# Kernel tuning notes

Measured on AMD Instinct MI355X. Metric: run time of the kernel, lower is better.

The kernel has to match this reference:

```python
import jax, jax.numpy as jnp
import numpy as np

N = 50000   # nodes
E = 400000  # edges
IN = 128    # in_dim
D = 32      # out_dim (per head)
H = 8       # heads
M = 8       # random features; must equal H so m//heads == 1 (see notes)


def setup_inputs() -> dict:
    key = jax.random.key(0)
    ks = jax.random.split(key, 8)
    x = jax.random.normal(ks[0], (N, IN), dtype=jnp.float32)
    edge_index = jax.random.randint(ks[1], (2, E), 0, N, dtype=jnp.int32)
    edge_sign = (2 * jax.random.randint(ks[2], (E,), 0, 2, dtype=jnp.int32) - 1)  # {-1,+1}
    s = 1.0 / np.sqrt(IN)
    Wq = jax.random.normal(ks[3], (IN, H * D), dtype=jnp.float32) * s
    Wk = jax.random.normal(ks[4], (IN, H * D), dtype=jnp.float32) * s
    Wv = jax.random.normal(ks[5], (IN, H * D), dtype=jnp.float32) * s
    RF = jax.random.normal(ks[6], (D, M), dtype=jnp.float32)    # iSKDE buffer
    RF_q = jax.random.normal(ks[7], (D, M), dtype=jnp.float32)  # frozen param
    return {"x": x, "Wq": Wq, "Wk": Wk, "Wv": Wv, "RF": RF, "RF_q": RF_q,
            "edge_index": edge_index, "edge_sign": edge_sign}


def reference(x, Wq, Wk, Wv, RF, RF_q, edge_index, edge_sign):
    n = x.shape[0]
    q = (x @ Wq).reshape(n, H, D)
    k = (x @ Wk).reshape(n, H, D)
    v = (x @ Wv).reshape(n, H, D)

    # ---- iSKDE.build (torch.no_grad) over N*H 'nodes' (rows of k_flat) ----
    k_flat = k.reshape(n * H, D)
    proj = k_flat @ RF                                  # [N*H, M]
    phi = (jnp.cos(proj) + jnp.sin(proj)).reshape(n * H, H, M // H)  # [N*H, H, 1]

    src, dst = edge_index[0], edge_index[1]
    posf = (edge_sign == 1).astype(x.dtype)             # [E]
    negf = (edge_sign == -1).astype(x.dtype)

    deg_pos = jnp.zeros((n * H, H), x.dtype).at[dst].add(jnp.broadcast_to(posf[:, None], (E, H)))
    deg_neg = jnp.zeros((n * H, H), x.dtype).at[dst].add(jnp.broadcast_to(negf[:, None], (E, H)))
    phi_src = phi[src]                                  # [E, H, 1]
    pk_pos = jnp.zeros((n * H, H, M // H), x.dtype).at[dst].add(phi_src * posf[:, None, None])
    pk_neg = jnp.zeros((n * H, H, M // H), x.dtype).at[dst].add(phi_src * negf[:, None, None])
    # build is under torch.no_grad -> constants w.r.t. autodiff
    pk_pos, pk_neg, deg_pos, deg_neg = map(jax.lax.stop_gradient, (pk_pos, pk_neg, deg_pos, deg_neg))

    # ---- random-feature query map ----
    qproj = q @ RF_q                                    # [N, H, M]
    q_phi = jnp.cos(qproj) + jnp.sin(qproj)

    # ---- iSKDE.forward on edges (row=src queries, col=dst keys) ----
    q_e = q_phi[src]                                    # [E, H, M]
    num_pos = (q_e * pk_pos[dst]).sum(-1)               # [E,H,M]*[E,H,1] -> [E,H]
    num_neg = (q_e * pk_neg[dst]).sum(-1)
    den_pos = jnp.maximum(deg_pos[dst], 1.0)            # clamp_min(1)
    den_neg = jnp.maximum(deg_neg[dst], 1.0)

    attn = jax.nn.softmax(num_pos / den_pos, axis=-1) - jax.nn.softmax(num_neg / den_neg, axis=-1)
    # dropout p=0.0 -> identity

    messages = v[dst] * attn[..., None]                 # [E, H, D]
    out = jnp.zeros((n, H, D), x.dtype).at[src].add(messages)
    return out.reshape(n, -1)
```

## Files before the change

kernel.cpp:

```cpp
#include <hip/hip_runtime.h>

constexpr int N_NODES = 50000;
constexpr int E_EDGES = 400000;
constexpr int IN_DIM  = 128;
constexpr int HD      = 256;
constexpr int H_HEADS = 8;
constexpr int D_HEAD  = 32;
constexpr int M_FEAT  = 8;
constexpr int K_NODES = N_NODES / H_HEADS;
constexpr int CAP     = 48;
constexpr int BUCKET_BLOCKS = (E_EDGES + 255) / 256;
constexpr int XFORM_BLOCKS  = N_NODES / 16;
constexpr int ZERO_INT4     = (2 * N_NODES) / 4;
constexpr int ZERO_BLOCKS   = (ZERO_INT4 + 255) / 256;

typedef __attribute__((ext_vector_type(8))) short bf16x8;
typedef __attribute__((ext_vector_type(4))) float f32x4;

__device__ inline short to_bf16(float f) {
    unsigned u = __builtin_bit_cast(unsigned, f);
    u += 0x7FFFu + ((u >> 16) & 1u);
    return (short)(u >> 16);
}
__device__ inline float bf16f(short h) {
    return __builtin_bit_cast(float, (unsigned)(unsigned short)h << 16);
}

__global__ __launch_bounds__(256) void prep_kernel(
    const float* __restrict__ Wq, const float* __restrict__ Wk,
    const float* __restrict__ Wv, const float* __restrict__ RF,
    const float* __restrict__ RFq,
    unsigned short* __restrict__ WqTh, unsigned short* __restrict__ WqTl,
    unsigned short* __restrict__ WkTh, unsigned short* __restrict__ WkTl,
    unsigned short* __restrict__ WvT, int* __restrict__ cnts)
{
    const int b = blockIdx.x;
    const int t = threadIdx.x;
    if (b < 64) {
        const bool isQ = (b < 32);
        const int idx = (isQ ? b : b - 32) * 256 + t;
        const int d = idx >> 6;
        const int c = idx & 63;
        const int hj = c >> 3, m = c & 7;
        const float* W = isQ ? Wq : Wk;
        const float* R = isQ ? RFq : RF;
        float acc = 0.f;
        #pragma unroll
        for (int dd = 0; dd < D_HEAD; ++dd)
            acc = fmaf(W[d * HD + hj * D_HEAD + dd], R[dd * M_FEAT + m], acc);
        const short h = to_bf16(acc);
        const short l = to_bf16(acc - bf16f(h));
        (isQ ? WqTh : WkTh)[c * IN_DIM + d] = (unsigned short)h;
        (isQ ? WqTl : WkTl)[c * IN_DIM + d] = (unsigned short)l;
    } else if (b < 192) {
        const int idx = (b - 64) * 256 + t;
        const int n = idx >> 7;
        const int d = idx & 127;
        WvT[idx] = (unsigned short)to_bf16(Wv[d * HD + n]);
    } else {
        const int idx = (b - 192) * 256 + t;
        if (idx < ZERO_INT4)
            ((int4*)cnts)[idx] = make_int4(0, 0, 0, 0);
    }
}

__global__ __launch_bounds__(256, 4) void main_kernel(
    const int* __restrict__ src, const int* __restrict__ dst,
    const int* __restrict__ sign,
    int* __restrict__ srcCnt, unsigned short* __restrict__ srcBucket,
    int* __restrict__ dstCnt, unsigned* __restrict__ dstBucket,
    const float* __restrict__ x, const unsigned short* __restrict__ WvT,
    const unsigned short* __restrict__ WqTh, const unsigned short* __restrict__ WqTl,
    const unsigned short* __restrict__ WkTh, const unsigned short* __restrict__ WkTl,
    unsigned short* __restrict__ Vb, float* __restrict__ Sq, float* __restrict__ Phi)
{
    if (blockIdx.x < BUCKET_BLOCKS) {
        const int e = blockIdx.x * 256 + threadIdx.x;
        if (e >= E_EDGES) return;
        const int s = src[e];
        const int d = dst[e];
        const unsigned sb = (sign[e] == 1) ? 0x80000000u : 0u;
        const int ss = atomicAdd(&srcCnt[s], 1);
        const int ds = atomicAdd(&dstCnt[d], 1);
        if (ss < CAP) srcBucket[(size_t)s * CAP + ss] = (unsigned short)d;
        if (ds < CAP) dstBucket[(size_t)d * CAP + ds] = (unsigned)s | sb;
        return;
    }

    const int r0   = (blockIdx.x - BUCKET_BLOCKS) * 16;
    const int w    = threadIdx.x >> 6;
    const int lane = threadIdx.x & 63;
    const int m    = lane & 15;
    const int quad = lane >> 4;

    bf16x8 Ah[4], Al[4];
    const float* xrow = x + (size_t)(r0 + m) * IN_DIM;
    #pragma unroll
    for (int t = 0; t < 4; ++t) {
        const float4 a = *(const float4*)(xrow + t * 32 + quad * 8);
        const float4 b = *(const float4*)(xrow + t * 32 + quad * 8 + 4);
        float vals[8] = {a.x, a.y, a.z, a.w, b.x, b.y, b.z, b.w};
        bf16x8 fh, fl;
        #pragma unroll
        for (int e = 0; e < 8; ++e) {
            const short hh = to_bf16(vals[e]);
            fh[e] = hh;
            fl[e] = to_bf16(vals[e] - bf16f(hh));
        }
        Ah[t] = fh; Al[t] = fl;
    }

    const unsigned short* bp = WvT + (size_t)m * IN_DIM + quad * 8;
    #pragma unroll
    for (int ii = 0; ii < 2; ++ii) {
        bf16x8 Bv[8];
        #pragma unroll
        for (int i = 0; i < 2; ++i) {
            const unsigned short* bc =
                bp + (size_t)(w * 4 + ii * 2 + i) * 16 * IN_DIM;
            #pragma unroll
            for (int t = 0; t < 4; ++t)
                Bv[i * 4 + t] = *(const bf16x8*)(bc + t * 32);
        }
        #pragma unroll
        for (int i = 0; i < 2; ++i) {
            const int ct = w * 4 + ii * 2 + i;
            f32x4 acc = {0.f, 0.f, 0.f, 0.f};
            #pragma unroll
            for (int t = 0; t < 4; ++t)
                acc = __builtin_amdgcn_mfma_f32_16x16x32_bf16(Ah[t], Bv[i * 4 + t], acc, 0, 0, 0);
            #pragma unroll
            for (int r = 0; r < 4; ++r)
                Vb[(size_t)(r0 + quad * 4 + r) * HD + ct * 16 + m] =
                    (unsigned short)to_bf16(acc[r]);
        }
    }

    {
        const int c = w * 16 + m;
        const unsigned short* bh = WqTh + (size_t)c * IN_DIM + quad * 8;
        const unsigned short* bl = WqTl + (size_t)c * IN_DIM + quad * 8;
        bf16x8 Bh[4], Bl[4];
        #pragma unroll
        for (int t = 0; t < 4; ++t) {
            Bh[t] = *(const bf16x8*)(bh + t * 32);
            Bl[t] = *(const bf16x8*)(bl + t * 32);
        }
        f32x4 acc1 = {0.f, 0.f, 0.f, 0.f};
        f32x4 acc2 = {0.f, 0.f, 0.f, 0.f};
        #pragma unroll
        for (int t = 0; t < 4; ++t) {
            acc1 = __builtin_amdgcn_mfma_f32_16x16x32_bf16(Ah[t], Bh[t], acc1, 0, 0, 0);
            acc2 = __builtin_amdgcn_mfma_f32_16x16x32_bf16(Al[t], Bh[t], acc2, 0, 0, 0);
        }
        #pragma unroll
        for (int t = 0; t < 4; ++t)
            acc1 = __builtin_amdgcn_mfma_f32_16x16x32_bf16(Ah[t], Bl[t], acc1, 0, 0, 0);
        #pragma unroll
        for (int r = 0; r < 4; ++r) {
            const float pv = acc1[r] + acc2[r];
            float tv = __cosf(pv) + __sinf(pv);
            tv += __shfl_xor(tv, 1);
            tv += __shfl_xor(tv, 2);
            tv += __shfl_xor(tv, 4);
            if ((lane & 7) == 0) {
                const int h = w * 2 + (m >> 3);
                Sq[(r0 + quad * 4 + r) * H_HEADS + h] = tv;
            }
        }
    }

    if (r0 < K_NODES) {
        const int c = w * 16 + m;
        const unsigned short* bh = WkTh + (size_t)c * IN_DIM + quad * 8;
        const unsigned short* bl = WkTl + (size_t)c * IN_DIM + quad * 8;
        bf16x8 Bh[4], Bl[4];
        #pragma unroll
        for (int t = 0; t < 4; ++t) {
            Bh[t] = *(const bf16x8*)(bh + t * 32);
            Bl[t] = *(const bf16x8*)(bl + t * 32);
        }
        f32x4 acc1 = {0.f, 0.f, 0.f, 0.f};
        f32x4 acc2 = {0.f, 0.f, 0.f, 0.f};
        #pragma unroll
        for (int t = 0; t < 4; ++t) {
            acc1 = __builtin_amdgcn_mfma_f32_16x16x32_bf16(Ah[t], Bh[t], acc1, 0, 0, 0);
            acc2 = __builtin_amdgcn_mfma_f32_16x16x32_bf16(Al[t], Bh[t], acc2, 0, 0, 0);
        }
        #pragma unroll
        for (int t = 0; t < 4; ++t)
            acc1 = __builtin_amdgcn_mfma_f32_16x16x32_bf16(Ah[t], Bl[t], acc1, 0, 0, 0);
        #pragma unroll
        for (int r = 0; r < 4; ++r) {
            const int row = r0 + quad * 4 + r;
            if (row < K_NODES) {
                const float pv = acc1[r] + acc2[r];
                Phi[(size_t)row * 64 + c] = __cosf(pv) + __sinf(pv);
            }
        }
    }
}

__global__ __launch_bounds__(256) void pk_kernel(
    const int* __restrict__ dstCnt, const unsigned* __restrict__ dstBucket,
    const float* __restrict__ Phi, float* __restrict__ PK)
{
    const int t = blockIdx.x * 256 + threadIdx.x;
    if (t >= N_NODES * H_HEADS) return;
    const int d = t >> 3;
    const int h = t & 7;
    int deg = dstCnt[d];
    if (deg > CAP) deg = CAP;

    float accp = 0.f, accn = 0.f;
    int cp = 0, cn = 0;
    for (int i = 0; i < deg; ++i) {
        const unsigned entry = dstBucket[(size_t)d * CAP + i];
        const float phi = Phi[(int)(entry & 0x7FFFFFFFu) * H_HEADS + h];
        if (entry & 0x80000000u) { accp += phi; ++cp; }
        else                     { accn += phi; ++cn; }
    }
    float2 pn;
    pn.x = accp / fmaxf((float)cp, 1.0f);
    pn.y = accn / fmaxf((float)cn, 1.0f);
    ((float2*)PK)[d * 8 + h] = pn;
}

__global__ __launch_bounds__(256) void accum_kernel(
    const int* __restrict__ srcCnt, const unsigned short* __restrict__ srcBucket,
    const float* __restrict__ Sq, const float* __restrict__ PK,
    const unsigned short* __restrict__ Vb, float* __restrict__ out)
{
    const int s = blockIdx.x * 4 + (threadIdx.x >> 6);
    const int lane = threadIdx.x & 63;
    const int j = lane >> 3;
    const int h = lane & 7;
    const int myhead = lane >> 3;

    int deg = srcCnt[s];
    if (deg > CAP) deg = CAP;
    const float sq = Sq[s * H_HEADS + h];

    float4 acc = make_float4(0.f, 0.f, 0.f, 0.f);
    const ushort4* __restrict__ V4 = (const ushort4*)Vb;
    const float2* __restrict__ PK2 = (const float2*)PK;

    for (int base = 0; base < deg; base += 8) {
        const int idx = base + j;
        const bool act = (idx < deg);
        const int dj = act ? (int)srcBucket[s * CAP + idx] : 0;

        const float2 pn = PK2[dj * 8 + h];
        const float np = sq * pn.x;
        const float nn = sq * pn.y;

        float mp = np, mn = nn;
        mp = fmaxf(mp, __shfl_xor(mp, 1)); mn = fmaxf(mn, __shfl_xor(mn, 1));
        mp = fmaxf(mp, __shfl_xor(mp, 2)); mn = fmaxf(mn, __shfl_xor(mn, 2));
        mp = fmaxf(mp, __shfl_xor(mp, 4)); mn = fmaxf(mn, __shfl_xor(mn, 4));
        float ep = __expf(np - mp), en = __expf(nn - mn);
        float sp = ep, sn = en;
        sp += __shfl_xor(sp, 1); sn += __shfl_xor(sn, 1);
        sp += __shfl_xor(sp, 2); sn += __shfl_xor(sn, 2);
        sp += __shfl_xor(sp, 4); sn += __shfl_xor(sn, 4);
        float a = ep / sp - en / sn;
        if (!act) a = 0.f;

        int   dd[8];
        float av[8];
        #pragma unroll
        for (int jj = 0; jj < 8; ++jj) {
            dd[jj] = __shfl(dj, jj * 8);
            av[jj] = __shfl(a,  jj * 8 + myhead);
        }
        ushort4 vv[8];
        #pragma unroll
        for (int jj = 0; jj < 8; ++jj)
            vv[jj] = V4[dd[jj] * 64 + lane];
        #pragma unroll
        for (int jj = 0; jj < 8; ++jj) {
            acc.x = fmaf(bf16f((short)vv[jj].x), av[jj], acc.x);
            acc.y = fmaf(bf16f((short)vv[jj].y), av[jj], acc.y);
            acc.z = fmaf(bf16f((short)vv[jj].z), av[jj], acc.z);
            acc.w = fmaf(bf16f((short)vv[jj].w), av[jj], acc.w);
        }
    }
    ((float4*)out)[s * 64 + lane] = acc;
}

extern "C" void kernel_launch(void* const* d_in, const int* in_sizes, int n_in,
                              void* d_out, int out_size, void* d_ws, size_t ws_size,
                              hipStream_t stream) {
    const float* x   = (const float*)d_in[0];
    const float* Wq  = (const float*)d_in[1];
    const float* Wk  = (const float*)d_in[2];
    const float* Wv  = (const float*)d_in[3];
    const float* RF  = (const float*)d_in[4];
    const float* RFq = (const float*)d_in[5];
    const int* eidx  = (const int*)d_in[6];
    const int* esign = (const int*)d_in[7];
    const int* src = eidx;
    const int* dst = eidx + E_EDGES;
    float* out = (float*)d_out;

    float* ws      = (float*)d_ws;
    unsigned short* Vb = (unsigned short*)ws;
    float* Sq      = ws + (size_t)N_NODES * HD / 2;
    float* Phi     = Sq + (size_t)N_NODES * H_HEADS;
    float* PK      = Phi + (size_t)K_NODES * 64;
    int* srcCnt    = (int*)(PK + (size_t)N_NODES * 16);
    int* dstCnt    = srcCnt + N_NODES;
    unsigned short* srcBucket = (unsigned short*)(dstCnt + N_NODES);
    unsigned* dstBucket = (unsigned*)(srcBucket + (size_t)N_NODES * CAP);
    unsigned short* WqTh = (unsigned short*)(dstBucket + (size_t)N_NODES * CAP);
    unsigned short* WqTl = WqTh + 64 * IN_DIM;
    unsigned short* WkTh = WqTl + 64 * IN_DIM;
    unsigned short* WkTl = WkTh + 64 * IN_DIM;
    unsigned short* WvT  = WkTl + 64 * IN_DIM;

    prep_kernel<<<192 + ZERO_BLOCKS, 256, 0, stream>>>(
        Wq, Wk, Wv, RF, RFq, WqTh, WqTl, WkTh, WkTl, WvT, srcCnt);
    main_kernel<<<BUCKET_BLOCKS + XFORM_BLOCKS, 256, 0, stream>>>(
        src, dst, esign, srcCnt, srcBucket, dstCnt, dstBucket,
        x, WvT, WqTh, WqTl, WkTh, WkTl, Vb, Sq, Phi);
    pk_kernel<<<(N_NODES * H_HEADS + 255) / 256, 256, 0, stream>>>(
        dstCnt, dstBucket, Phi, PK);
    accum_kernel<<<N_NODES / 4, 256, 0, stream>>>(
        srcCnt, srcBucket, Sq, PK, Vb, out);
}
```

Baseline: 226.0 us.

## Give each wave its own 16-row tile and put transform blocks before bucket blocks

Before, the four waves of a transform block shared 16 rows and split the output columns, so each wave converted the same x rows to bf16 hi/lo. Now each wave owns 16 rows and loops over all column tiles for V, Q and K, so x is loaded and split once per row while weight loads are repeated per wave. The transform blocks are also placed ahead of the bucketing blocks in the grid, which changes when the MFMA-heavy and atomic-heavy work is scheduled. Cost: four times fewer transform blocks, more serial work per wave, and redundant weight fetches that depend on cache hits.

```diff
diff --git a/kernel.cpp b/kernel.cpp
--- a/kernel.cpp
+++ b/kernel.cpp
@@ -10,7 +10,8 @@
 constexpr int K_NODES = N_NODES / H_HEADS;
 constexpr int CAP     = 48;
 constexpr int BUCKET_BLOCKS = (E_EDGES + 255) / 256;
-constexpr int XFORM_BLOCKS  = N_NODES / 16;
+constexpr int XFORM_BLOCKS  = (N_NODES + 63) / 64;
+constexpr int MAIN_BLOCKS   = XFORM_BLOCKS + BUCKET_BLOCKS;
 constexpr int ZERO_INT4     = (2 * N_NODES) / 4;
 constexpr int ZERO_BLOCKS   = (ZERO_INT4 + 255) / 256;
 
@@ -74,8 +75,8 @@
     const unsigned short* __restrict__ WkTh, const unsigned short* __restrict__ WkTl,
     unsigned short* __restrict__ Vb, float* __restrict__ Sq, float* __restrict__ Phi)
 {
-    if (blockIdx.x < BUCKET_BLOCKS) {
-        const int e = blockIdx.x * 256 + threadIdx.x;
+    if (blockIdx.x >= XFORM_BLOCKS) {
+        const int e = (blockIdx.x - XFORM_BLOCKS) * 256 + threadIdx.x;
         if (e >= E_EDGES) return;
         const int s = src[e];
         const int d = dst[e];
@@ -87,9 +88,10 @@
         return;
     }
 
-    const int r0   = (blockIdx.x - BUCKET_BLOCKS) * 16;
     const int w    = threadIdx.x >> 6;
     const int lane = threadIdx.x & 63;
+    const int r0   = blockIdx.x * 64 + w * 16;
+    if (r0 >= N_NODES) return;
     const int m    = lane & 15;
     const int quad = lane >> 4;
 
@@ -111,33 +113,37 @@
     }
 
     const unsigned short* bp = WvT + (size_t)m * IN_DIM + quad * 8;
-    #pragma unroll
-    for (int ii = 0; ii < 2; ++ii) {
-        bf16x8 Bv[8];
-        #pragma unroll
-        for (int i = 0; i < 2; ++i) {
-            const unsigned short* bc =
-                bp + (size_t)(w * 4 + ii * 2 + i) * 16 * IN_DIM;
-            #pragma unroll
-            for (int t = 0; t < 4; ++t)
-                Bv[i * 4 + t] = *(const bf16x8*)(bc + t * 32);
-        }
-        #pragma unroll
-        for (int i = 0; i < 2; ++i) {
-            const int ct = w * 4 + ii * 2 + i;
-            f32x4 acc = {0.f, 0.f, 0.f, 0.f};
-            #pragma unroll
-            for (int t = 0; t < 4; ++t)
-                acc = __builtin_amdgcn_mfma_f32_16x16x32_bf16(Ah[t], Bv[i * 4 + t], acc, 0, 0, 0);
-            #pragma unroll
-            for (int r = 0; r < 4; ++r)
-                Vb[(size_t)(r0 + quad * 4 + r) * HD + ct * 16 + m] =
-                    (unsigned short)to_bf16(acc[r]);
-        }
-    }
-
-    {
-        const int c = w * 16 + m;
+    #pragma unroll 1
+    for (int g = 0; g < 4; ++g) {
+        #pragma unroll
+        for (int ii = 0; ii < 2; ++ii) {
+            bf16x8 Bv[8];
+            #pragma unroll
+            for (int i = 0; i < 2; ++i) {
+                const unsigned short* bc =
+                    bp + (size_t)(g * 4 + ii * 2 + i) * 16 * IN_DIM;
+                #pragma unroll
+                for (int t = 0; t < 4; ++t)
+                    Bv[i * 4 + t] = *(const bf16x8*)(bc + t * 32);
+            }
+            #pragma unroll
+            for (int i = 0; i < 2; ++i) {
+                const int ct = g * 4 + ii * 2 + i;
+                f32x4 acc = {0.f, 0.f, 0.f, 0.f};
+                #pragma unroll
+                for (int t = 0; t < 4; ++t)
+                    acc = __builtin_amdgcn_mfma_f32_16x16x32_bf16(Ah[t], Bv[i * 4 + t], acc, 0, 0, 0);
+                #pragma unroll
+                for (int r = 0; r < 4; ++r)
+                    Vb[(size_t)(r0 + quad * 4 + r) * HD + ct * 16 + m] =
+                        (unsigned short)to_bf16(acc[r]);
+            }
+        }
+    }
+
+    #pragma unroll 1
+    for (int ct = 0; ct < 4; ++ct) {
+        const int c = ct * 16 + m;
         const unsigned short* bh = WqTh + (size_t)c * IN_DIM + quad * 8;
         const unsigned short* bl = WqTl + (size_t)c * IN_DIM + quad * 8;
         bf16x8 Bh[4], Bl[4];
@@ -164,38 +170,41 @@
             tv += __shfl_xor(tv, 2);
             tv += __shfl_xor(tv, 4);
             if ((lane & 7) == 0) {
-                const int h = w * 2 + (m >> 3);
+                const int h = ct * 2 + (m >> 3);
                 Sq[(r0 + quad * 4 + r) * H_HEADS + h] = tv;
             }
         }
     }
 
     if (r0 < K_NODES) {
-        const int c = w * 16 + m;
-        const unsigned short* bh = WkTh + (size_t)c * IN_DIM + quad * 8;
-        const unsigned short* bl = WkTl + (size_t)c * IN_DIM + quad * 8;
-        bf16x8 Bh[4], Bl[4];
-        #pragma unroll
-        for (int t = 0; t < 4; ++t) {
-            Bh[t] = *(const bf16x8*)(bh + t * 32);
-            Bl[t] = *(const bf16x8*)(bl + t * 32);
-        }
-        f32x4 acc1 = {0.f, 0.f, 0.f, 0.f};
-        f32x4 acc2 = {0.f, 0.f, 0.f, 0.f};
-        #pragma unroll
-        for (int t = 0; t < 4; ++t) {
-            acc1 = __builtin_amdgcn_mfma_f32_16x16x32_bf16(Ah[t], Bh[t], acc1, 0, 0, 0);
-            acc2 = __builtin_amdgcn_mfma_f32_16x16x32_bf16(Al[t], Bh[t], acc2, 0, 0, 0);
-        }
-        #pragma unroll
-        for (int t = 0; t < 4; ++t)
-            acc1 = __builtin_amdgcn_mfma_f32_16x16x32_bf16(Ah[t], Bl[t], acc1, 0, 0, 0);
-        #pragma unroll
-        for (int r = 0; r < 4; ++r) {
-            const int row = r0 + quad * 4 + r;
-            if (row < K_NODES) {
-                const float pv = acc1[r] + acc2[r];
-                Phi[(size_t)row * 64 + c] = __cosf(pv) + __sinf(pv);
+        #pragma unroll 1
+        for (int ct = 0; ct < 4; ++ct) {
+            const int c = ct * 16 + m;
+            const unsigned short* bh = WkTh + (size_t)c * IN_DIM + quad * 8;
+            const unsigned short* bl = WkTl + (size_t)c * IN_DIM + quad * 8;
+            bf16x8 Bh[4], Bl[4];
+            #pragma unroll
+            for (int t = 0; t < 4; ++t) {
+                Bh[t] = *(const bf16x8*)(bh + t * 32);
+                Bl[t] = *(const bf16x8*)(bl + t * 32);
+            }
+            f32x4 acc1 = {0.f, 0.f, 0.f, 0.f};
+            f32x4 acc2 = {0.f, 0.f, 0.f, 0.f};
+            #pragma unroll
+            for (int t = 0; t < 4; ++t) {
+                acc1 = __builtin_amdgcn_mfma_f32_16x16x32_bf16(Ah[t], Bh[t], acc1, 0, 0, 0);
+                acc2 = __builtin_amdgcn_mfma_f32_16x16x32_bf16(Al[t], Bh[t], acc2, 0, 0, 0);
+            }
+            #pragma unroll
+            for (int t = 0; t < 4; ++t)
+                acc1 = __builtin_amdgcn_mfma_f32_16x16x32_bf16(Ah[t], Bl[t], acc1, 0, 0, 0);
+            #pragma unroll
+            for (int r = 0; r < 4; ++r) {
+                const int row = r0 + quad * 4 + r;
+                if (row < K_NODES) {
+                    const float pv = acc1[r] + acc2[r];
+                    Phi[(size_t)row * 64 + c] = __cosf(pv) + __sinf(pv);
+                }
             }
         }
     }
@@ -320,7 +329,7 @@
 
     prep_kernel<<<192 + ZERO_BLOCKS, 256, 0, stream>>>(
         Wq, Wk, Wv, RF, RFq, WqTh, WqTl, WkTh, WkTl, WvT, srcCnt);
-    main_kernel<<<BUCKET_BLOCKS + XFORM_BLOCKS, 256, 0, stream>>>(
+    main_kernel<<<MAIN_BLOCKS, 256, 0, stream>>>(
         src, dst, esign, srcCnt, srcBucket, dstCnt, dstBucket,
         x, WvT, WqTh, WqTl, WkTh, WkTl, Vb, Sq, Phi);
     pk_kernel<<<(N_NODES * H_HEADS + 255) / 256, 256, 0, stream>>>(
```

Result: faster. 207.0 us (-8.4%).
